# Optimization experiments

Measured on AMD Instinct MI355X. Metric: run time of the kernel, lower is better.

The kernel has to match this reference:

```python
import jax, jax.numpy as jnp
import numpy as np
from jax.scipy.special import logsumexp

B, T, NT = 8192, 512, 7  # batch, seq_len, num_tags


def setup_inputs() -> dict:
    key = jax.random.key(0)
    k1, k2, k3, k4, k5 = jax.random.split(key, 5)
    emissions = jax.random.normal(k1, (B, T, NT), dtype=jnp.float32)
    labels = jax.random.randint(k2, (B, T), 0, NT)
    mask = jnp.ones((B, T), dtype=jnp.int32)  # first timestep must be on (torchcrf requirement)
    # CRF parameters (torchcrf initializes uniform in [-0.1, 0.1])
    start_transitions = jax.random.uniform(k3, (NT,), minval=-0.1, maxval=0.1, dtype=jnp.float32)
    end_transitions = jax.random.uniform(k4, (NT,), minval=-0.1, maxval=0.1, dtype=jnp.float32)
    transitions = jax.random.uniform(k5, (NT, NT), minval=-0.1, maxval=0.1, dtype=jnp.float32)
    return {
        "emissions": emissions,
        "labels": labels,
        "mask": mask,
        "start_transitions": start_transitions,
        "end_transitions": end_transitions,
        "transitions": transitions,
    }


def _crf_neg_log_likelihood(emissions, labels, mask, start_transitions, end_transitions, transitions):
    # emissions: (B, T, NT); labels: (B, T) int; mask: (B, T) {0,1}
    b, t, nt = emissions.shape
    maskf = mask.astype(emissions.dtype)
    batch_idx = jnp.arange(b)

    # ---- numerator: score of the gold tag path (fully vectorized) ----
    tags = jnp.where(labels < 0, 0, labels)  # labels[labels < 0] = 0 in the torch module
    num = start_transitions[tags[:, 0]] + emissions[batch_idx, 0, tags[:, 0]]
    trans_score = transitions[tags[:, :-1], tags[:, 1:]]                      # (B, T-1)
    emit_score = jnp.take_along_axis(emissions[:, 1:], tags[:, 1:, None], axis=2)[..., 0]  # (B, T-1)
    num = num + jnp.sum((trans_score + emit_score) * maskf[:, 1:], axis=1)
    seq_ends = jnp.sum(mask, axis=1).astype(jnp.int32) - 1                     # (B,)
    last_tags = tags[batch_idx, seq_ends]
    num = num + end_transitions[last_tags]

    # ---- denominator: log partition via forward-algorithm scan over time ----
    init_score = start_transitions[None, :] + emissions[:, 0]  # (B, NT)

    def step(score, inp):
        emit_t, m_t = inp  # (B, NT), (B,)
        # broadcast: score over previous tag, transitions (prev, next), emissions at next tag
        next_score = logsumexp(score[:, :, None] + transitions[None, :, :] + emit_t[:, None, :], axis=1)
        score = jnp.where(m_t[:, None] > 0, next_score, score)
        return score, None

    xs = (jnp.moveaxis(emissions[:, 1:], 1, 0), mask[:, 1:].T)  # (T-1, B, NT), (T-1, B)
    final_score, _ = jax.lax.scan(step, init_score, xs)
    den = logsumexp(final_score + end_transitions[None, :], axis=1)  # (B,)

    # torchcrf default reduction='sum'; module returns loss = -crf(...)
    return jnp.sum(den - num)


def reference(emissions, labels, mask, start_transitions, end_transitions, transitions):
    return _crf_neg_log_likelihood(emissions, labels, mask, start_transitions, end_transitions, transitions)
```

## Files before the change

kernel.cpp:

```cpp
#include <hip/hip_runtime.h>


#define Bsz 8192
#define Tsz 512
#define NTG 7
#define NCH 32
#define CS  16
#define RPB 8
#define THB 256

__device__ __forceinline__ float rfl(float x) {
    return __int_as_float(__builtin_amdgcn_readfirstlane(__float_as_int(x)));
}

__device__ __forceinline__ float wsumf(float x) {
#pragma unroll
    for (int m = 1; m < 64; m <<= 1) x += __shfl_xor(x, m, 64);
    return x;
}
__device__ __forceinline__ int wsumi(int x) {
#pragma unroll
    for (int m = 1; m < 64; m <<= 1) x += __shfl_xor(x, m, 64);
    return x;
}
__device__ __forceinline__ float wmaxf(float x) {
#pragma unroll
    for (int m = 1; m < 64; m <<= 1) x = fmaxf(x, __shfl_xor(x, m, 64));
    return x;
}

__global__ __launch_bounds__(THB) void crf_fused_kernel(
    const float* __restrict__ em, const int* __restrict__ labels,
    const int* __restrict__ mask, const float* __restrict__ startT,
    const float* __restrict__ endT, const float* __restrict__ trans,
    float* __restrict__ blockpart)
{
    __shared__ float ldsM[THB * 49 + 20];
    __shared__ float ldsLs[THB];
    __shared__ float ldsNum[THB];
    __shared__ int   ldsCnt[THB];
    __shared__ float transS[52];
    __shared__ float rowval[RPB];

    const int t  = threadIdx.x;
    const int c  = t & (NCH - 1);
    const int rl = t >> 5;
    const int r  = blockIdx.x * RPB + rl;

    if (t < 49) transS[t] = trans[t];
    __syncthreads();

    float W[49];
#pragma unroll
    for (int k = 0; k < 49; ++k) W[k] = rfl(__expf(trans[k]));

    float M[49];
#pragma unroll
    for (int k = 0; k < 49; ++k) M[k] = 0.0f;
#pragma unroll
    for (int i = 0; i < 7; ++i) M[i * 7 + i] = 1.0f;

    float logscale = 0.0f, num = 0.0f;
    int cnt = 0;

    const int t0 = c * CS;
    const float* emr  = em + (size_t)r * (Tsz * NTG) + (size_t)t0 * NTG;
    const int*   labr = labels + r * Tsz + t0;
    const int*   mskr = mask   + r * Tsz + t0;

    int lprev = 0;
    if (c > 0) { lprev = labr[-1]; if (lprev < 0) lprev = 0; }

#pragma unroll
    for (int g = 0; g < CS / 4; ++g) {
        float4 ev[7];
        const float4* ep = (const float4*)(emr + g * 28);
#pragma unroll
        for (int q = 0; q < 7; ++q) ev[q] = ep[q];
        const float* eraw = (const float*)&ev[0];

        int4 lab4 = *(const int4*)(labr + g * 4);
        int4 msk4 = *(const int4*)(mskr + g * 4);
        int labs[4] = {lab4.x, lab4.y, lab4.z, lab4.w};
        int msks[4] = {msk4.x, msk4.y, msk4.z, msk4.w};

#pragma unroll
        for (int s = 0; s < 4; ++s) {
            const int tt = t0 + g * 4 + s;
            int lc = labs[s]; if (lc < 0) lc = 0;
            const float mf = (float)msks[s];
            cnt += msks[s];

            float esel = eraw[s * 7 + 0];
#pragma unroll
            for (int j = 1; j < 7; ++j) esel = (lc == j) ? eraw[s * 7 + j] : esel;

            if (tt == 0) {
                num += startT[lc] + esel;
            } else {
                num += mf * (transS[lprev * 7 + lc] + esel);
                if (msks[s] > 0) {
                    float e[7];
#pragma unroll
                    for (int j = 0; j < 7; ++j) e[j] = __expf(eraw[s * 7 + j]);
#pragma unroll
                    for (int i = 0; i < 7; ++i) {
                        float tmp[7];
#pragma unroll
                        for (int j = 0; j < 7; ++j) tmp[j] = 0.0f;
#pragma unroll
                        for (int k = 0; k < 7; ++k) {
                            const float mik = M[i * 7 + k];
#pragma unroll
                            for (int j = 0; j < 7; ++j)
                                tmp[j] = fmaf(mik, W[k * 7 + j], tmp[j]);
                        }
#pragma unroll
                        for (int j = 0; j < 7; ++j) M[i * 7 + j] = tmp[j] * e[j];
                    }
                }
            }
            lprev = lc;
        }
        if (g & 1) {
            float mx = 1e-30f;
#pragma unroll
            for (int k = 0; k < 49; ++k) mx = fmaxf(mx, M[k]);
            const float inv = 1.0f / mx;
#pragma unroll
            for (int k = 0; k < 49; ++k) M[k] *= inv;
            logscale += __logf(mx);
        }
    }

#pragma unroll
    for (int k = 0; k < 49; ++k) ldsM[t * 49 + k] = M[k];
    ldsLs[t]  = logscale;
    ldsNum[t] = num;
    ldsCnt[t] = cnt;
    __syncthreads();

    const int lane = t & 63;
    const int wv   = t >> 6;
    const int idiv = lane / 7;

    for (int rr = 0; rr < 2; ++rr) {
        const int rl2 = wv * 2 + rr;
        const int r2  = blockIdx.x * RPB + rl2;

        float v = 0.0f;
        if (lane < 7) v = __expf(startT[lane] + em[(size_t)r2 * (Tsz * NTG) + lane]);
        float ls = 0.0f;

        for (int cc = 0; cc < NCH; ++cc) {
            const float Mk = ldsM[(rl2 * NCH + cc) * 49 + lane];
            const float vi = __shfl(v, idiv, 64);
            float p = (lane < 49) ? vi * Mk : 0.0f;
            p += __shfl_down(p, 28, 64);
            p += __shfl_down(p, 14, 64);
            p += __shfl_down(p, 7, 64);
            const float mx = wmaxf(p);
            v = p * (1.0f / mx);
            ls += __logf(mx);
        }

        float lsA  = (lane < NCH) ? ldsLs[rl2 * NCH + lane]  : 0.0f;
        float numA = (lane < NCH) ? ldsNum[rl2 * NCH + lane] : 0.0f;
        int   cntA = (lane < NCH) ? ldsCnt[rl2 * NCH + lane] : 0;
        ls += wsumf(lsA);
        float numt = wsumf(numA);
        int   cntt = wsumi(cntA);

        float term = (lane < 7) ? v * __expf(endT[lane]) : 0.0f;
        const float den = ls + __logf(wsumf(term));

        int se = cntt - 1; if (se < 0) se = 0;
        int lt = labels[r2 * Tsz + se]; if (lt < 0) lt = 0;
        numt += endT[lt];

        if (lane == 0) rowval[rl2] = den - numt;
    }
    __syncthreads();

    if (t == 0) {
        float s = 0.0f;
#pragma unroll
        for (int k = 0; k < RPB; ++k) s += rowval[k];
        blockpart[blockIdx.x] = s;
    }
}

__global__ __launch_bounds__(256) void crf_reduce_kernel(
    const float* __restrict__ part, float* __restrict__ out)
{
    const int t = threadIdx.x;
    float s = part[t] + part[t + 256] + part[t + 512] + part[t + 768];
    __shared__ float red[256];
    red[t] = s;
    __syncthreads();
    for (int off = 128; off > 0; off >>= 1) {
        if (t < off) red[t] += red[t + off];
        __syncthreads();
    }
    if (t == 0) out[0] = red[0];
}

extern "C" void kernel_launch(void* const* d_in, const int* in_sizes, int n_in,
                              void* d_out, int out_size, void* d_ws, size_t ws_size,
                              hipStream_t stream) {
    const float* em     = (const float*)d_in[0];
    const int*   labels = (const int*)d_in[1];
    const int*   mask   = (const int*)d_in[2];
    const float* startT = (const float*)d_in[3];
    const float* endT   = (const float*)d_in[4];
    const float* trans  = (const float*)d_in[5];
    float* out = (float*)d_out;
    float* blockpart = (float*)d_ws;
    (void)in_sizes; (void)n_in; (void)out_size; (void)ws_size;

    crf_fused_kernel<<<Bsz / RPB, THB, 0, stream>>>(
        em, labels, mask, startT, endT, trans, blockpart);
    crf_reduce_kernel<<<1, 256, 0, stream>>>(blockpart, out);
}
```

Measured before the change: 272.2 us.

## Replace serial per-row chunk combine with log-depth tree of matrix products

Instead of each wavefront sequentially applying 32 chunk transfer matrices to a vector via shuffles, chunk matrices are combined pairwise in a 5-level tree through LDS, with one thread per row finishing with the start vector and end transitions. This is meant to cut the serial 32-step shuffle chain in the combine phase. In exchange, each tree level costs a full 7x7 matrix-matrix product, 49 LDS writes and reads, and a block barrier, and most threads sit idle at the higher levels. The per-thread emission loads are also unpacked into a flat register array, which is cosmetic.

Result: faster. 237.8 us (-12.6%).

```diff
diff --git a/kernel.cpp b/kernel.cpp
--- a/kernel.cpp
+++ b/kernel.cpp
@@ -13,33 +13,17 @@
     return __int_as_float(__builtin_amdgcn_readfirstlane(__float_as_int(x)));
 }
 
-__device__ __forceinline__ float wsumf(float x) {
-#pragma unroll
-    for (int m = 1; m < 64; m <<= 1) x += __shfl_xor(x, m, 64);
-    return x;
-}
-__device__ __forceinline__ int wsumi(int x) {
-#pragma unroll
-    for (int m = 1; m < 64; m <<= 1) x += __shfl_xor(x, m, 64);
-    return x;
-}
-__device__ __forceinline__ float wmaxf(float x) {
-#pragma unroll
-    for (int m = 1; m < 64; m <<= 1) x = fmaxf(x, __shfl_xor(x, m, 64));
-    return x;
-}
-
 __global__ __launch_bounds__(THB) void crf_fused_kernel(
     const float* __restrict__ em, const int* __restrict__ labels,
     const int* __restrict__ mask, const float* __restrict__ startT,
     const float* __restrict__ endT, const float* __restrict__ trans,
     float* __restrict__ blockpart)
 {
-    __shared__ float ldsM[THB * 49 + 20];
+    __shared__ float ldsM[THB * 49];
     __shared__ float ldsLs[THB];
     __shared__ float ldsNum[THB];
     __shared__ int   ldsCnt[THB];
-    __shared__ float transS[52];
+    __shared__ float transS[49];
     __shared__ float rowval[RPB];
 
     const int t  = threadIdx.x;
@@ -73,12 +57,14 @@
 
 #pragma unroll
     for (int g = 0; g < CS / 4; ++g) {
-        float4 ev[7];
+        float er[28];
         const float4* ep = (const float4*)(emr + g * 28);
 #pragma unroll
-        for (int q = 0; q < 7; ++q) ev[q] = ep[q];
-        const float* eraw = (const float*)&ev[0];
-
+        for (int q = 0; q < 7; ++q) {
+            float4 v = ep[q];
+            er[4 * q + 0] = v.x; er[4 * q + 1] = v.y;
+            er[4 * q + 2] = v.z; er[4 * q + 3] = v.w;
+        }
         int4 lab4 = *(const int4*)(labr + g * 4);
         int4 msk4 = *(const int4*)(mskr + g * 4);
         int labs[4] = {lab4.x, lab4.y, lab4.z, lab4.w};
@@ -91,9 +77,9 @@
             const float mf = (float)msks[s];
             cnt += msks[s];
 
-            float esel = eraw[s * 7 + 0];
-#pragma unroll
-            for (int j = 1; j < 7; ++j) esel = (lc == j) ? eraw[s * 7 + j] : esel;
+            float esel = er[s * 7 + 0];
+#pragma unroll
+            for (int j = 1; j < 7; ++j) esel = (lc == j) ? er[s * 7 + j] : esel;
 
             if (tt == 0) {
                 num += startT[lc] + esel;
@@ -102,7 +88,7 @@
                 if (msks[s] > 0) {
                     float e[7];
 #pragma unroll
-                    for (int j = 0; j < 7; ++j) e[j] = __expf(eraw[s * 7 + j]);
+                    for (int j = 0; j < 7; ++j) e[j] = __expf(er[s * 7 + j]);
 #pragma unroll
                     for (int i = 0; i < 7; ++i) {
                         float tmp[7];
@@ -133,52 +119,84 @@
         }
     }
 
-#pragma unroll
-    for (int k = 0; k < 49; ++k) ldsM[t * 49 + k] = M[k];
-    ldsLs[t]  = logscale;
     ldsNum[t] = num;
     ldsCnt[t] = cnt;
-    __syncthreads();
-
-    const int lane = t & 63;
-    const int wv   = t >> 6;
-    const int idiv = lane / 7;
-
-    for (int rr = 0; rr < 2; ++rr) {
-        const int rl2 = wv * 2 + rr;
-        const int r2  = blockIdx.x * RPB + rl2;
-
-        float v = 0.0f;
-        if (lane < 7) v = __expf(startT[lane] + em[(size_t)r2 * (Tsz * NTG) + lane]);
-        float ls = 0.0f;
-
-        for (int cc = 0; cc < NCH; ++cc) {
-            const float Mk = ldsM[(rl2 * NCH + cc) * 49 + lane];
-            const float vi = __shfl(v, idiv, 64);
-            float p = (lane < 49) ? vi * Mk : 0.0f;
-            p += __shfl_down(p, 28, 64);
-            p += __shfl_down(p, 14, 64);
-            p += __shfl_down(p, 7, 64);
-            const float mx = wmaxf(p);
-            v = p * (1.0f / mx);
-            ls += __logf(mx);
-        }
-
-        float lsA  = (lane < NCH) ? ldsLs[rl2 * NCH + lane]  : 0.0f;
-        float numA = (lane < NCH) ? ldsNum[rl2 * NCH + lane] : 0.0f;
-        int   cntA = (lane < NCH) ? ldsCnt[rl2 * NCH + lane] : 0;
-        ls += wsumf(lsA);
-        float numt = wsumf(numA);
-        int   cntt = wsumi(cntA);
-
-        float term = (lane < 7) ? v * __expf(endT[lane]) : 0.0f;
-        const float den = ls + __logf(wsumf(term));
-
-        int se = cntt - 1; if (se < 0) se = 0;
-        int lt = labels[r2 * Tsz + se]; if (lt < 0) lt = 0;
-        numt += endT[lt];
-
-        if (lane == 0) rowval[rl2] = den - numt;
+
+    float ls = logscale;
+    ldsLs[t] = ls;
+#pragma unroll
+    for (int L = 1; L <= 5; ++L) {
+        const int half = 1 << (L - 1);
+        const int m    = (1 << L) - 1;
+        const bool isB = (c & m) == half;
+        const bool isA = (c & m) == 0;
+
+        if (isB) {
+#pragma unroll
+            for (int k = 0; k < 49; ++k) ldsM[t * 49 + k] = M[k];
+            ldsLs[t] = ls;
+        }
+        __syncthreads();
+        if (isA) {
+            float Bm[49];
+#pragma unroll
+            for (int k = 0; k < 49; ++k) Bm[k] = ldsM[(t + half) * 49 + k];
+#pragma unroll
+            for (int i = 0; i < 7; ++i) {
+                float tmp[7];
+#pragma unroll
+                for (int j = 0; j < 7; ++j) tmp[j] = 0.0f;
+#pragma unroll
+                for (int k = 0; k < 7; ++k) {
+                    const float mik = M[i * 7 + k];
+#pragma unroll
+                    for (int j = 0; j < 7; ++j)
+                        tmp[j] = fmaf(mik, Bm[k * 7 + j], tmp[j]);
+                }
+#pragma unroll
+                for (int j = 0; j < 7; ++j) M[i * 7 + j] = tmp[j];
+            }
+            float mx = 1e-30f;
+#pragma unroll
+            for (int k = 0; k < 49; ++k) mx = fmaxf(mx, M[k]);
+            const float inv = 1.0f / mx;
+#pragma unroll
+            for (int k = 0; k < 49; ++k) M[k] *= inv;
+            ls += __logf(mx) + ldsLs[t + half];
+        }
+    }
+    __syncthreads();
+
+    if (c == 0) {
+        const float* em0 = em + (size_t)r * (Tsz * NTG);
+        float a0[7];
+#pragma unroll
+        for (int j = 0; j < 7; ++j) a0[j] = __expf(startT[j] + em0[j]);
+        float nv[7];
+#pragma unroll
+        for (int j = 0; j < 7; ++j) nv[j] = 0.0f;
+#pragma unroll
+        for (int i = 0; i < 7; ++i) {
+            const float ai = a0[i];
+#pragma unroll
+            for (int j = 0; j < 7; ++j)
+                nv[j] = fmaf(ai, M[i * 7 + j], nv[j]);
+        }
+        float dsum = 0.0f;
+#pragma unroll
+        for (int j = 0; j < 7; ++j) dsum += nv[j] * __expf(endT[j]);
+        const float den = ls + __logf(dsum);
+
+        float numT = 0.0f; int cntT = 0;
+        for (int q = 0; q < NCH; ++q) {
+            numT += ldsNum[rl * NCH + q];
+            cntT += ldsCnt[rl * NCH + q];
+        }
+        int se = cntT - 1; if (se < 0) se = 0;
+        int lt = labels[r * Tsz + se]; if (lt < 0) lt = 0;
+        numT += endT[lt];
+
+        rowval[rl] = den - numT;
     }
     __syncthreads();
 
```
